# Optimization experiments

Measured on AMD Instinct MI355X. Metric: run time of the kernel, lower is better.

The kernel has to match this reference:

```python
import jax, jax.numpy as jnp
import numpy as np

TINY = 1e-8
B, T, D = 128, 32, 400


def _offsets(T):
    offs, off = [], 0
    for lvl in range(T):
        offs.append(off)
        off += T - lvl
    return offs


def _inside_indices(T):
    # For level l, span start i (L = T - l spans), split k in [0, l):
    #   left child  = cell(offs[k] + i)             (span (i, level k))
    #   right child = cell(offs[l-k-1] + i + k + 1) (span (i+k+1, level l-k-1))
    offs = _offsets(T)
    out = {}
    for level in range(1, T):
        L = T - level
        lidx = np.empty((L, level), np.int32)
        ridx = np.empty((L, level), np.int32)
        for i in range(L):
            for k in range(level):
                lidx[i, k] = offs[k] + i
                ridx[i, k] = offs[level - k - 1] + i + k + 1
        out[level] = (jnp.asarray(lidx.reshape(-1)), jnp.asarray(ridx.reshape(-1)))
    return offs, out


def unit_norm(x):
    n = jnp.sqrt(jnp.sum(x * x, axis=-1, keepdims=True))
    return x / jnp.maximum(n, TINY)


def setup_inputs() -> dict:
    key = jax.random.key(0)
    ks = jax.random.split(key, 12)
    sc = 1.0 / np.sqrt(D).astype(np.float32)
    return {
        'x': jax.random.normal(ks[0], (B, T, D), jnp.float32),
        'w_leaf_h': jax.random.normal(ks[1], (D, D), jnp.float32) * sc,
        'b_leaf_h': jax.random.normal(ks[2], (D,), jnp.float32) * sc,
        'w_leaf_c': jax.random.normal(ks[3], (D, D), jnp.float32) * sc,
        'b_leaf_c': jax.random.normal(ks[4], (D,), jnp.float32) * sc,
        'u_lh': jax.random.normal(ks[5], (D, D), jnp.float32) * sc,
        'u_rh': jax.random.normal(ks[6], (D, D), jnp.float32) * sc,
        'b_h': jax.random.normal(ks[7], (D,), jnp.float32) * sc,
        'u_lc': jax.random.normal(ks[8], (D, D), jnp.float32) * sc,
        'u_rc': jax.random.normal(ks[9], (D, D), jnp.float32) * sc,
        'b_c': jax.random.normal(ks[10], (D,), jnp.float32) * sc,
        'w_score': jax.random.normal(ks[11], (D, D), jnp.float32) * sc,
    }


def reference(x, w_leaf_h, b_leaf_h, w_leaf_c, b_leaf_c,
              u_lh, u_rh, b_h, u_lc, u_rc, b_c, w_score):
    Bb, Tt, Dd = x.shape
    offs, idx = _inside_indices(Tt)
    ncells = Tt * (Tt + 1) // 2
    # leaf_transform + unit normalize
    h0 = unit_norm(jnp.tanh(x @ w_leaf_h + b_leaf_h))
    c0 = unit_norm(jnp.tanh(x @ w_leaf_c + b_leaf_c))
    ch = jnp.zeros((Bb, ncells, Dd), x.dtype).at[:, :Tt].set(h0)
    cc = jnp.zeros((Bb, ncells, Dd), x.dtype).at[:, :Tt].set(c0)
    cs = jnp.zeros((Bb, ncells, 1), x.dtype)
    for level in range(1, Tt):  # fixed structural loop over tree levels
        L, N = Tt - level, level
        lidx, ridx = idx[level]
        lh, rh = ch[:, lidx], ch[:, ridx]  # gather: [B, L*N, D]
        lc, rc = cc[:, lidx], cc[:, ridx]
        ls, rs = cs[:, lidx], cs[:, ridx]  # [B, L*N, 1]
        # compose
        h = jnp.tanh(lh @ u_lh + rh @ u_rh + b_h)
        c = jnp.tanh(lc @ u_lc + rc @ u_rc + b_c)
        # bilinear score + child scores, softmax over splits N
        s = jnp.einsum('bnd,de,bne->bn', lh, w_score, rh)[..., None] + ls + rs
        s = s.reshape(Bb, L, N, 1)
        p = jax.nn.softmax(s, axis=2)
        h_agg = unit_norm(jnp.sum(h.reshape(Bb, L, N, Dd) * p, axis=2))
        c_agg = unit_norm(jnp.sum(c.reshape(Bb, L, N, Dd) * p, axis=2))
        s_agg = jnp.sum(s * p, axis=2)
        off = offs[level]
        ch = ch.at[:, off:off + L].set(h_agg)
        cc = cc.at[:, off:off + L].set(c_agg)
        cs = cs.at[:, off:off + L].set(s_agg)
    return ch
```

## Files before the change

### kernel.cpp

```cpp
#include <hip/hip_runtime.h>
#include <hip/hip_bf16.h>
#include <stdint.h>


#define BB 128
#define TT 32
#define DD 400
#define NCELLS 528
#define NW 2000
#define KP 416

typedef __hip_bfloat16 bf16_t;
typedef __attribute__((ext_vector_type(8))) short s8v;
typedef __attribute__((ext_vector_type(4))) float f32x4;

__device__ __forceinline__ int offs_of(int v) { return v * TT - (v * (v - 1)) / 2; }

__device__ __forceinline__ float asf(uint32_t bits) {
    union { uint32_t i; float f; } v; v.i = bits; return v.f;
}
__device__ __forceinline__ uint16_t f2bf(float f) {
    union { float f; uint32_t i; } v; v.f = f;
    uint32_t x = v.i;
    return (uint16_t)((x + 0x7fffu + ((x >> 16) & 1u)) >> 16);
}

__device__ __forceinline__ void block_reduce2(float& a, float& b, float* sred) {
#pragma unroll
    for (int o = 32; o > 0; o >>= 1) { a += __shfl_down(a, o); b += __shfl_down(b, o); }
    int lane = threadIdx.x & 63, w = threadIdx.x >> 6;
    if (lane == 0) { sred[w] = a; sred[4 + w] = b; }
    __syncthreads();
    a = sred[0] + sred[1] + sred[2] + sred[3];
    b = sred[4] + sred[5] + sred[6] + sred[7];
    __syncthreads();
}

__global__ void pack_k(const float* __restrict__ u_lh, const float* __restrict__ u_rh,
                       const float* __restrict__ w_score, const float* __restrict__ u_lc,
                       const float* __restrict__ u_rc, const float* __restrict__ w_leaf_h,
                       const float* __restrict__ w_leaf_c, const float* __restrict__ x,
                       uint16_t* __restrict__ WT, uint16_t* __restrict__ WLT,
                       uint16_t* __restrict__ XB) {
    int idx = blockIdx.x * blockDim.x + threadIdx.x;
    const int nWT = NW * KP, nWLT = 800 * KP, nXB = 4096 * KP;
    if (idx < nWT) {
        int n = idx / KP, k = idx - n * KP;
        float v = 0.f;
        if (k < DD) {
            const float* src = (n < 400) ? u_lh : (n < 800) ? u_rh : (n < 1200) ? w_score
                               : (n < 1600) ? u_lc : u_rc;
            v = src[k * DD + (n % 400)];
        }
        WT[idx] = f2bf(v);
    } else if (idx < nWT + nWLT) {
        int q = idx - nWT; int n = q / KP, k = q - n * KP;
        float v = 0.f;
        if (k < DD) v = (n < 400) ? w_leaf_h[k * DD + n] : w_leaf_c[k * DD + (n - 400)];
        WLT[q] = f2bf(v);
    } else if (idx < nWT + nWLT + nXB) {
        int q = idx - nWT - nWLT; int r = q / KP, k = q - r * KP;
        XB[q] = f2bf(k < DD ? x[(size_t)r * DD + k] : 0.f);
    }
}

__global__ __launch_bounds__(256)
void tgemm_k(const uint16_t* __restrict__ HB, const uint16_t* __restrict__ CB,
             const uint16_t* __restrict__ WT,
             uint16_t* __restrict__ LP, uint16_t* __restrict__ RP, uint16_t* __restrict__ G,
             float* __restrict__ PREout, int mode, int Lcur, int cellbase) {
    __shared__ short As[128][40];
    __shared__ short Ws[80][40];
    const int t = threadIdx.x, lane = t & 63, w = t >> 6;
    const int n0 = blockIdx.x * 80;
    const int tile_m = blockIdx.y * 128;
    const bool cside = (mode == 0) && (n0 >= 1200);

    const int arow_l = t >> 2, asub = t & 3;
    const uint16_t* aptr[2];
#pragma unroll
    for (int p = 0; p < 2; p++) {
        int gr = tile_m + arow_l + 64 * p;
        const uint16_t* base;
        if (mode == 1) {
            base = HB + (size_t)gr * KP;
        } else {
            int rb = gr / Lcur, ri = gr - rb * Lcur;
            base = cside ? CB + (size_t)(rb * 32 + ri) * DD
                         : HB + (size_t)(rb * NCELLS + cellbase + ri) * DD;
        }
        aptr[p] = base + asub * 8;
    }
    const uint16_t* wptr0 = WT + (size_t)(n0 + (t >> 2)) * KP + (t & 3) * 8;
    const uint16_t* wptr1 = WT + (size_t)(n0 + 64 + (t >> 2)) * KP + (t & 3) * 8;

    const int frow = lane & 15, kcol = (lane >> 4) * 8;
    f32x4 acc[2][5];
#pragma unroll
    for (int mi = 0; mi < 2; mi++)
#pragma unroll
        for (int ni = 0; ni < 5; ni++) acc[mi][ni] = (f32x4)(0.f);

    for (int k0 = 0; k0 < KP; k0 += 32) {
        s8v av0 = *(const s8v*)(aptr[0] + k0);
        s8v av1 = *(const s8v*)(aptr[1] + k0);
        s8v wv0 = *(const s8v*)(wptr0 + k0);
        s8v wv1;
        if (t < 64) wv1 = *(const s8v*)(wptr1 + k0);
        __syncthreads();
        *(s8v*)&As[arow_l][asub * 8] = av0;
        *(s8v*)&As[arow_l + 64][asub * 8] = av1;
        *(s8v*)&Ws[t >> 2][(t & 3) * 8] = wv0;
        if (t < 64) *(s8v*)&Ws[64 + (t >> 2)][(t & 3) * 8] = wv1;
        __syncthreads();
        s8v a0 = *(const s8v*)&As[32 * w + frow][kcol];
        s8v a1 = *(const s8v*)&As[32 * w + 16 + frow][kcol];
#pragma unroll
        for (int ni = 0; ni < 5; ni++) {
            s8v bv = *(const s8v*)&Ws[16 * ni + frow][kcol];
            acc[0][ni] = __builtin_amdgcn_mfma_f32_16x16x32_bf16(a0, bv, acc[0][ni], 0, 0, 0);
            acc[1][ni] = __builtin_amdgcn_mfma_f32_16x16x32_bf16(a1, bv, acc[1][ni], 0, 0, 0);
        }
    }

    const int seg = n0 / 400, ncb = n0 % 400;
    uint16_t* tb = (seg == 2) ? G : (seg == 0 || seg == 3) ? LP : RP;
    const int slot = (seg >= 3) ? 1 : 0;
#pragma unroll
    for (int mi = 0; mi < 2; mi++) {
        int rbase = tile_m + 32 * w + 16 * mi + 4 * (lane >> 4);
#pragma unroll
        for (int i = 0; i < 4; i++) {
            int gr = rbase + i;
            if (mode == 1) {
                float* o = PREout + (size_t)gr * 800 + n0 + frow;
#pragma unroll
                for (int ni = 0; ni < 5; ni++) o[16 * ni] = acc[mi][ni][i];
            } else {
                int rb = gr / Lcur, ri = gr - rb * Lcur;
                size_t row = (size_t)(rb * NCELLS + cellbase + ri);
                if (seg == 2) {
                    uint16_t* o = tb + row * 400 + ncb + frow;
#pragma unroll
                    for (int ni = 0; ni < 5; ni++) o[16 * ni] = f2bf(acc[mi][ni][i]);
                } else {
                    uint16_t* o = tb + row * 800 + 2 * (ncb + frow) + slot;
#pragma unroll
                    for (int ni = 0; ni < 5; ni++) o[32 * ni] = f2bf(acc[mi][ni][i]);
                }
            }
        }
    }
}

__global__ __launch_bounds__(256)
void leaf_norm_k(const float* __restrict__ PRE, const float* __restrict__ blh,
                 const float* __restrict__ blc, float* __restrict__ Hchart,
                 uint16_t* __restrict__ HB, uint16_t* __restrict__ CB,
                 float* __restrict__ cs) {
    const int r = blockIdx.x;
    const int b = r >> 5, tt = r & 31;
    const int t = threadIdx.x;
    const int d = t * 2;
    float th0 = 0, th1 = 0, tc0 = 0, tc1 = 0;
    if (d < DD) {
        const float* p = PRE + (size_t)r * 800;
        th0 = tanhf(p[d] + blh[d]);
        th1 = tanhf(p[d + 1] + blh[d + 1]);
        tc0 = tanhf(p[400 + d] + blc[d]);
        tc1 = tanhf(p[400 + d + 1] + blc[d + 1]);
    }
    __shared__ float sred[8];
    float nh = th0 * th0 + th1 * th1, nc = tc0 * tc0 + tc1 * tc1;
    block_reduce2(nh, nc, sred);
    float rh = 1.f / fmaxf(sqrtf(nh), 1e-8f);
    float rc = 1.f / fmaxf(sqrtf(nc), 1e-8f);
    if (d < DD) {
        size_t ho = (size_t)(b * NCELLS + tt) * DD + d;
        float h0 = th0 * rh, h1 = th1 * rh, c0 = tc0 * rc, c1 = tc1 * rc;
        Hchart[ho] = h0; Hchart[ho + 1] = h1;
        *(uint32_t*)(HB + ho) = (uint32_t)f2bf(h0) | ((uint32_t)f2bf(h1) << 16);
        *(uint32_t*)(CB + (size_t)(b * 32 + tt) * DD + d) =
            (uint32_t)f2bf(c0) | ((uint32_t)f2bf(c1) << 16);
    }
    if (t == 0) cs[b * NCELLS + tt] = 0.f;
}

__global__ __launch_bounds__(256)
void level_k(float* __restrict__ Hchart, uint16_t* __restrict__ HB,
             uint16_t* __restrict__ CB, float* __restrict__ cs,
             const uint16_t* __restrict__ LP, const uint16_t* __restrict__ RP,
             const uint16_t* __restrict__ G,
             const float* __restrict__ b_h, const float* __restrict__ b_c, int level) {
    const int L = TT - level, N = level;
    const int blk = blockIdx.x;
    const int b = blk / L, i = blk - b * L;
    const int cell = offs_of(level) + i;
    const int t = threadIdx.x, lane = t & 63, w = t >> 6;
    __shared__ float sh_s[32], sh_p[32];
    __shared__ float sred[8];

    for (int k = w; k < N; k += 4) {
        int lcell = offs_of(k) + i;
        int rcell = offs_of(level - k - 1) + i + k + 1;
        const uint32_t* g = (const uint32_t*)(G + (size_t)(b * NCELLS + lcell) * DD);
        const uint32_t* hr = (const uint32_t*)(HB + (size_t)(b * NCELLS + rcell) * DD);
        float s = 0.f;
        for (int d2 = lane; d2 < 200; d2 += 64) {
            uint32_t gv = g[d2], hv = hr[d2];
            s += asf(gv << 16) * asf(hv << 16)
               + asf(gv & 0xffff0000u) * asf(hv & 0xffff0000u);
        }
#pragma unroll
        for (int o = 32; o > 0; o >>= 1) s += __shfl_down(s, o);
        if (lane == 0) sh_s[k] = s + cs[b * NCELLS + lcell] + cs[b * NCELLS + rcell];
    }
    __syncthreads();

    if (t == 0) {
        float m = -1e30f;
        for (int k = 0; k < N; k++) m = fmaxf(m, sh_s[k]);
        float sum = 0.f;
        for (int k = 0; k < N; k++) { float e = expf(sh_s[k] - m); sh_p[k] = e; sum += e; }
        float inv = 1.f / sum, sagg = 0.f;
        for (int k = 0; k < N; k++) { sh_p[k] *= inv; sagg += sh_p[k] * sh_s[k]; }
        cs[b * NCELLS + cell] = sagg;
    }
    __syncthreads();

    float ha0 = 0, ha1 = 0, ca0 = 0, ca1 = 0;
    const int d = t * 2;
    if (d < DD) {
        const float bh0 = b_h[d], bh1 = b_h[d + 1], bc0 = b_c[d], bc1 = b_c[d + 1];
        const uint16_t* lpb = LP + (size_t)(b * NCELLS) * 800 + 2 * d;
        const uint16_t* rpb = RP + (size_t)(b * NCELLS) * 800 + 2 * d;
        for (int k = 0; k < N; k++) {
            float p = sh_p[k];
            int lcell = offs_of(k) + i;
            int rcell = offs_of(level - k - 1) + i + k + 1;
            uint2 lv = *(const uint2*)(lpb + (size_t)lcell * 800);
            uint2 rv = *(const uint2*)(rpb + (size_t)rcell * 800);
            ha0 += p * tanhf(asf(lv.x << 16) + asf(rv.x << 16) + bh0);
            ca0 += p * tanhf(asf(lv.x & 0xffff0000u) + asf(rv.x & 0xffff0000u) + bc0);
            ha1 += p * tanhf(asf(lv.y << 16) + asf(rv.y << 16) + bh1);
            ca1 += p * tanhf(asf(lv.y & 0xffff0000u) + asf(rv.y & 0xffff0000u) + bc1);
        }
    }
    float nh = ha0 * ha0 + ha1 * ha1, nc = ca0 * ca0 + ca1 * ca1;
    block_reduce2(nh, nc, sred);
    float rh = 1.f / fmaxf(sqrtf(nh), 1e-8f);
    float rc = 1.f / fmaxf(sqrtf(nc), 1e-8f);
    if (d < DD) {
        float h0 = ha0 * rh, h1 = ha1 * rh, c0 = ca0 * rc, c1 = ca1 * rc;
        size_t ho = (size_t)(b * NCELLS + cell) * DD + d;
        Hchart[ho] = h0; Hchart[ho + 1] = h1;
        *(uint32_t*)(HB + ho) = (uint32_t)f2bf(h0) | ((uint32_t)f2bf(h1) << 16);
        *(uint32_t*)(CB + (size_t)(b * 32 + i) * DD + d) =
            (uint32_t)f2bf(c0) | ((uint32_t)f2bf(c1) << 16);
    }
}

extern "C" void kernel_launch(void* const* d_in, const int* in_sizes, int n_in,
                              void* d_out, int out_size, void* d_ws, size_t ws_size,
                              hipStream_t stream) {
    const float* x        = (const float*)d_in[0];
    const float* w_leaf_h = (const float*)d_in[1];
    const float* b_leaf_h = (const float*)d_in[2];
    const float* w_leaf_c = (const float*)d_in[3];
    const float* b_leaf_c = (const float*)d_in[4];
    const float* u_lh     = (const float*)d_in[5];
    const float* u_rh     = (const float*)d_in[6];
    const float* b_h      = (const float*)d_in[7];
    const float* u_lc     = (const float*)d_in[8];
    const float* u_rc     = (const float*)d_in[9];
    const float* b_c      = (const float*)d_in[10];
    const float* w_score  = (const float*)d_in[11];
    float* Hchart = (float*)d_out;

    const size_t PL = (size_t)BB * NCELLS * DD;
    char* p = (char*)d_ws;
    uint16_t* LP = (uint16_t*)p; p += 2 * PL * sizeof(uint16_t);
    uint16_t* RP = (uint16_t*)p; p += 2 * PL * sizeof(uint16_t);
    uint16_t* G  = (uint16_t*)p; p += PL * sizeof(uint16_t);
    uint16_t* HB = (uint16_t*)p; p += PL * sizeof(uint16_t) + 64;
    uint16_t* CB = (uint16_t*)p; p += (size_t)BB * 32 * DD * sizeof(uint16_t) + 64;
    float* CS    = (float*)p;    p += (size_t)BB * NCELLS * sizeof(float);
    uint16_t* WT = (uint16_t*)p; p += (size_t)NW * KP * sizeof(uint16_t);
    float* PRE    = (float*)LP;
    uint16_t* WLT = RP;
    uint16_t* XB  = RP + (size_t)800 * KP;

    {
        int total = NW * KP + 800 * KP + 4096 * KP;
        pack_k<<<(total + 255) / 256, 256, 0, stream>>>(u_lh, u_rh, w_score, u_lc, u_rc,
                                                        w_leaf_h, w_leaf_c, x, WT, WLT, XB);
    }
    tgemm_k<<<dim3(10, 32), 256, 0, stream>>>(XB, nullptr, WLT, nullptr, nullptr, nullptr,
                                              PRE, 1, 32, 0);
    leaf_norm_k<<<BB * TT, 256, 0, stream>>>(PRE, b_leaf_h, b_leaf_c, Hchart, HB, CB, CS);
    tgemm_k<<<dim3(25, 32), 256, 0, stream>>>(HB, CB, WT, LP, RP, G, nullptr, 0, 32, 0);

    int off = TT;
    for (int level = 1; level < TT; ++level) {
        int L = TT - level;
        level_k<<<BB * L, 256, 0, stream>>>(Hchart, HB, CB, CS, LP, RP, G, b_h, b_c, level);
        if (level < TT - 1) {
            tgemm_k<<<dim3(25, L), 256, 0, stream>>>(HB, CB, WT, LP, RP, G, nullptr, 0, L, off);
        }
        off += L;
    }
}
```

Baseline: 1.611 ms.

## Enlarge GEMM M-tile to 256 rows and use fast exp2-based tanh/softmax

Doubles the GEMM row tile from 128 to 256 so each block reuses its weight tile over four MFMA row-fragments per wave, halves the grid and adds bounds guards for partial tiles. It also replaces tanhf and expf in the leaf and level kernels with hardware exp2/rcp approximations. The larger tile raises register and LDS use and leaves fewer blocks at small levels, and the fast tanh is slightly less accurate and may overflow for large inputs.

```diff
diff --git a/kernel.cpp b/kernel.cpp
--- a/kernel.cpp
+++ b/kernel.cpp
@@ -23,6 +23,11 @@
     union { float f; uint32_t i; } v; v.f = f;
     uint32_t x = v.i;
     return (uint16_t)((x + 0x7fffu + ((x >> 16) & 1u)) >> 16);
+}
+
+__device__ __forceinline__ float tanh_fast(float x) {
+    float e = __builtin_amdgcn_exp2f(x * 2.8853900817779268f);
+    return 1.f - 2.f * __builtin_amdgcn_rcpf(e + 1.f);
 }
 
 __device__ __forceinline__ void block_reduce2(float& a, float& b, float* sred) {
@@ -69,18 +74,20 @@
              const uint16_t* __restrict__ WT,
              uint16_t* __restrict__ LP, uint16_t* __restrict__ RP, uint16_t* __restrict__ G,
              float* __restrict__ PREout, int mode, int Lcur, int cellbase) {
-    __shared__ short As[128][40];
+    __shared__ short As[256][40];
     __shared__ short Ws[80][40];
     const int t = threadIdx.x, lane = t & 63, w = t >> 6;
     const int n0 = blockIdx.x * 80;
-    const int tile_m = blockIdx.y * 128;
+    const int tile_m = blockIdx.y * 256;
     const bool cside = (mode == 0) && (n0 >= 1200);
+    const int Mtot = (mode == 1) ? 4096 : 128 * Lcur;
 
     const int arow_l = t >> 2, asub = t & 3;
-    const uint16_t* aptr[2];
-#pragma unroll
-    for (int p = 0; p < 2; p++) {
+    const uint16_t* aptr[4];
+#pragma unroll
+    for (int p = 0; p < 4; p++) {
         int gr = tile_m + arow_l + 64 * p;
+        if (gr >= Mtot) gr = 0;
         const uint16_t* base;
         if (mode == 1) {
             base = HB + (size_t)gr * KP;
@@ -95,31 +102,35 @@
     const uint16_t* wptr1 = WT + (size_t)(n0 + 64 + (t >> 2)) * KP + (t & 3) * 8;
 
     const int frow = lane & 15, kcol = (lane >> 4) * 8;
-    f32x4 acc[2][5];
-#pragma unroll
-    for (int mi = 0; mi < 2; mi++)
+    f32x4 acc[4][5];
+#pragma unroll
+    for (int mi = 0; mi < 4; mi++)
 #pragma unroll
         for (int ni = 0; ni < 5; ni++) acc[mi][ni] = (f32x4)(0.f);
 
     for (int k0 = 0; k0 < KP; k0 += 32) {
-        s8v av0 = *(const s8v*)(aptr[0] + k0);
-        s8v av1 = *(const s8v*)(aptr[1] + k0);
+        s8v av[4];
+#pragma unroll
+        for (int p = 0; p < 4; p++) av[p] = *(const s8v*)(aptr[p] + k0);
         s8v wv0 = *(const s8v*)(wptr0 + k0);
         s8v wv1;
         if (t < 64) wv1 = *(const s8v*)(wptr1 + k0);
         __syncthreads();
-        *(s8v*)&As[arow_l][asub * 8] = av0;
-        *(s8v*)&As[arow_l + 64][asub * 8] = av1;
+#pragma unroll
+        for (int p = 0; p < 4; p++) *(s8v*)&As[arow_l + 64 * p][asub * 8] = av[p];
         *(s8v*)&Ws[t >> 2][(t & 3) * 8] = wv0;
         if (t < 64) *(s8v*)&Ws[64 + (t >> 2)][(t & 3) * 8] = wv1;
         __syncthreads();
-        s8v a0 = *(const s8v*)&As[32 * w + frow][kcol];
-        s8v a1 = *(const s8v*)&As[32 * w + 16 + frow][kcol];
+        s8v a[4];
+#pragma unroll
+        for (int mi = 0; mi < 4; mi++)
+            a[mi] = *(const s8v*)&As[64 * w + 16 * mi + frow][kcol];
 #pragma unroll
         for (int ni = 0; ni < 5; ni++) {
             s8v bv = *(const s8v*)&Ws[16 * ni + frow][kcol];
-            acc[0][ni] = __builtin_amdgcn_mfma_f32_16x16x32_bf16(a0, bv, acc[0][ni], 0, 0, 0);
-            acc[1][ni] = __builtin_amdgcn_mfma_f32_16x16x32_bf16(a1, bv, acc[1][ni], 0, 0, 0);
+#pragma unroll
+            for (int mi = 0; mi < 4; mi++)
+                acc[mi][ni] = __builtin_amdgcn_mfma_f32_16x16x32_bf16(a[mi], bv, acc[mi][ni], 0, 0, 0);
         }
     }
 
@@ -127,11 +138,12 @@
     uint16_t* tb = (seg == 2) ? G : (seg == 0 || seg == 3) ? LP : RP;
     const int slot = (seg >= 3) ? 1 : 0;
 #pragma unroll
-    for (int mi = 0; mi < 2; mi++) {
-        int rbase = tile_m + 32 * w + 16 * mi + 4 * (lane >> 4);
+    for (int mi = 0; mi < 4; mi++) {
+        int rbase = tile_m + 64 * w + 16 * mi + 4 * (lane >> 4);
 #pragma unroll
         for (int i = 0; i < 4; i++) {
             int gr = rbase + i;
+            if (gr >= Mtot) continue;
             if (mode == 1) {
                 float* o = PREout + (size_t)gr * 800 + n0 + frow;
 #pragma unroll
@@ -165,10 +177,10 @@
     float th0 = 0, th1 = 0, tc0 = 0, tc1 = 0;
     if (d < DD) {
         const float* p = PRE + (size_t)r * 800;
-        th0 = tanhf(p[d] + blh[d]);
-        th1 = tanhf(p[d + 1] + blh[d + 1]);
-        tc0 = tanhf(p[400 + d] + blc[d]);
-        tc1 = tanhf(p[400 + d + 1] + blc[d + 1]);
+        th0 = tanh_fast(p[d] + blh[d]);
+        th1 = tanh_fast(p[d + 1] + blh[d + 1]);
+        tc0 = tanh_fast(p[400 + d] + blc[d]);
+        tc1 = tanh_fast(p[400 + d + 1] + blc[d + 1]);
     }
     __shared__ float sred[8];
     float nh = th0 * th0 + th1 * th1, nc = tc0 * tc0 + tc1 * tc1;
@@ -221,7 +233,10 @@
         float m = -1e30f;
         for (int k = 0; k < N; k++) m = fmaxf(m, sh_s[k]);
         float sum = 0.f;
-        for (int k = 0; k < N; k++) { float e = expf(sh_s[k] - m); sh_p[k] = e; sum += e; }
+        for (int k = 0; k < N; k++) {
+            float e = __builtin_amdgcn_exp2f((sh_s[k] - m) * 1.4426950408889634f);
+            sh_p[k] = e; sum += e;
+        }
         float inv = 1.f / sum, sagg = 0.f;
         for (int k = 0; k < N; k++) { sh_p[k] *= inv; sagg += sh_p[k] * sh_s[k]; }
         cs[b * NCELLS + cell] = sagg;
@@ -240,10 +255,10 @@
             int rcell = offs_of(level - k - 1) + i + k + 1;
             uint2 lv = *(const uint2*)(lpb + (size_t)lcell * 800);
             uint2 rv = *(const uint2*)(rpb + (size_t)rcell * 800);
-            ha0 += p * tanhf(asf(lv.x << 16) + asf(rv.x << 16) + bh0);
-            ca0 += p * tanhf(asf(lv.x & 0xffff0000u) + asf(rv.x & 0xffff0000u) + bc0);
-            ha1 += p * tanhf(asf(lv.y << 16) + asf(rv.y << 16) + bh1);
-            ca1 += p * tanhf(asf(lv.y & 0xffff0000u) + asf(rv.y & 0xffff0000u) + bc1);
+            ha0 += p * tanh_fast(asf(lv.x << 16) + asf(rv.x << 16) + bh0);
+            ca0 += p * tanh_fast(asf(lv.x & 0xffff0000u) + asf(rv.x & 0xffff0000u) + bc0);
+            ha1 += p * tanh_fast(asf(lv.y << 16) + asf(rv.y << 16) + bh1);
+            ca1 += p * tanh_fast(asf(lv.y & 0xffff0000u) + asf(rv.y & 0xffff0000u) + bc1);
         }
     }
     float nh = ha0 * ha0 + ha1 * ha1, nc = ca0 * ca0 + ca1 * ca1;
@@ -295,17 +310,18 @@
         pack_k<<<(total + 255) / 256, 256, 0, stream>>>(u_lh, u_rh, w_score, u_lc, u_rc,
                                                         w_leaf_h, w_leaf_c, x, WT, WLT, XB);
     }
-    tgemm_k<<<dim3(10, 32), 256, 0, stream>>>(XB, nullptr, WLT, nullptr, nullptr, nullptr,
+    tgemm_k<<<dim3(10, 16), 256, 0, stream>>>(XB, nullptr, WLT, nullptr, nullptr, nullptr,
                                               PRE, 1, 32, 0);
     leaf_norm_k<<<BB * TT, 256, 0, stream>>>(PRE, b_leaf_h, b_leaf_c, Hchart, HB, CB, CS);
-    tgemm_k<<<dim3(25, 32), 256, 0, stream>>>(HB, CB, WT, LP, RP, G, nullptr, 0, 32, 0);
+    tgemm_k<<<dim3(25, 16), 256, 0, stream>>>(HB, CB, WT, LP, RP, G, nullptr, 0, 32, 0);
 
     int off = TT;
     for (int level = 1; level < TT; ++level) {
         int L = TT - level;
         level_k<<<BB * L, 256, 0, stream>>>(Hchart, HB, CB, CS, LP, RP, G, b_h, b_c, level);
         if (level < TT - 1) {
-            tgemm_k<<<dim3(25, L), 256, 0, stream>>>(HB, CB, WT, LP, RP, G, nullptr, 0, L, off);
+            int mby = (128 * L + 255) / 256;
+            tgemm_k<<<dim3(25, mby), 256, 0, stream>>>(HB, CB, WT, LP, RP, G, nullptr, 0, L, off);
         }
         off += L;
     }
```

New measurement: 1.648 ms. 2.3% more time.
